# Performance work log

Measured on AMD Instinct MI355X. Metric: run time of the kernel, lower is better.

The kernel has to match this reference:

```python
import jax, jax.numpy as jnp
import numpy as np

EPS = 1e-7

def squash(t, axis=-1):
    sq = jnp.sum(jnp.square(t), axis=axis, keepdims=True)
    safe_norm = jnp.sqrt(sq + EPS)
    return t * (sq / (1.0 + sq)) / safe_norm


def setup_inputs() -> dict:
    key = jax.random.key(0)
    k1, k2 = jax.random.split(key)
    B, I, Din, N, D = 32, 1024, 32, 64, 32
    x = jax.random.normal(k1, (B, I, Din), dtype=jnp.float32)
    # glorot-ish scale ~ sqrt(2/(Din+D)) = 0.1767; use 0.1
    W = jax.random.normal(k2, (N, I, D, Din), dtype=jnp.float32) * 0.1
    return {"x": x, "W": W, "num_routing": 3}


def _infer(inputs_hat, logits):
    # softmax over the num_capsule axis (axis=1), matching tf.nn.softmax(logits, axis=1)
    route = jax.nn.softmax(logits, axis=1)                      # [B,N,1,I]
    routing = jnp.squeeze(jnp.matmul(route, inputs_hat), -2)    # [B,N,D]
    return squash(routing)


def reference(x, W, num_routing):
    # inputs_hat[b,n,i,d] = sum_k x[b,i,k] * W[n,i,d,k]
    inputs_hat = jnp.einsum('bik,nidk->bnid', x, W)             # [B,N,I,D]
    B, N, I, D = inputs_hat.shape
    ih_stop = jax.lax.stop_gradient(inputs_hat)
    logits = jnp.zeros((B, N, 1, I), dtype=inputs_hat.dtype)
    outputs = None
    for r in range(num_routing):
        if r == num_routing - 1:
            outputs = _infer(inputs_hat, logits)
        else:
            outputs = _infer(ih_stop, logits)
            # distances[b,n,1,i] = <outputs[b,n,:], ih_stop[b,n,i,:]>
            dist = jnp.matmul(outputs[:, :, None, :], jnp.swapaxes(ih_stop, -1, -2))
            logits = logits + dist
    return outputs
```

## Files before the change

kernel.cpp:

```cpp
#include <hip/hip_runtime.h>
#include <stdint.h>

#define II 1024
#define BBc 32
#define NN 64
#define DD 32
#define NDT 2048

__device__ __forceinline__ unsigned short f2bf(float f) {
  unsigned u = __float_as_uint(f);
  u += 0x7fffu + ((u >> 16) & 1u);
  return (unsigned short)(u >> 16);
}

__global__ __launch_bounds__(256) void k1_einsum(
    const float* __restrict__ x, const float* __restrict__ W,
    unsigned short* __restrict__ ih)
{
  __shared__ float xl[32][36];
  __shared__ float wl[8][256][4];
  const int t = threadIdx.x;
  const int i = blockIdx.x;
  const int half = blockIdx.y;
  const int ndg = t & 63;
  const int bg = t >> 6;
  const int b0 = bg * 8;

  {
    const int b = t >> 3, kq = (t & 7) * 4;
    const float4 v = *(const float4*)(x + ((size_t)b * II + i) * 32 + kq);
    xl[kq + 0][b] = v.x; xl[kq + 1][b] = v.y; xl[kq + 2][b] = v.z; xl[kq + 3][b] = v.w;
  }

  for (int p = 0; p < 4; ++p) {
    const int ndbase = half * 1024 + p * 256;
    __syncthreads();
#pragma unroll
    for (int it = 0; it < 8; ++it) {
      const int f = t + it * 256;
      const int kq = f & 7, nd = f >> 3;
      const int gnd = ndbase + nd;
      const int n = gnd >> 5, d = gnd & 31;
      const float4 v = *(const float4*)(W + (((size_t)n * II + i) * 32 + d) * 32 + kq * 4);
      *(float4*)&wl[kq][nd][0] = v;
    }
    __syncthreads();

    float acc[8][4] = {};
#pragma unroll
    for (int kq = 0; kq < 8; ++kq) {
      float wv[4][4];
#pragma unroll
      for (int q = 0; q < 4; ++q)
        *(float4*)wv[q] = *(const float4*)&wl[kq][ndg + 64 * q][0];
#pragma unroll
      for (int r = 0; r < 4; ++r) {
        const int k = kq * 4 + r;
        float xv[8];
        *(float4*)&xv[0] = *(const float4*)&xl[k][b0];
        *(float4*)&xv[4] = *(const float4*)&xl[k][b0 + 4];
#pragma unroll
        for (int bb = 0; bb < 8; ++bb)
#pragma unroll
          for (int q = 0; q < 4; ++q)
            acc[bb][q] += xv[bb] * wv[q][r];
      }
    }
#pragma unroll
    for (int bb = 0; bb < 8; ++bb) {
      const size_t rb = ((size_t)(b0 + bb) * II + i) * NDT + ndbase + ndg;
#pragma unroll
      for (int q = 0; q < 4; ++q)
        ih[rb + 64 * q] = f2bf(acc[bb][q]);
    }
  }
}

__global__ __launch_bounds__(256) void s0red(
    const unsigned short* __restrict__ ih, float* __restrict__ s0p)
{
  const int b = blockIdx.x, is = blockIdx.y;
  const int t = threadIdx.x;
  const unsigned short* base = ih + ((size_t)b * II + is * 64) * NDT + t * 8;
  float a[8] = {};
#pragma unroll 8
  for (int ii = 0; ii < 64; ++ii) {
    const uint4 v = *(const uint4*)(base + (size_t)ii * NDT);
    a[0] += __uint_as_float(v.x << 16); a[1] += __uint_as_float(v.x & 0xffff0000u);
    a[2] += __uint_as_float(v.y << 16); a[3] += __uint_as_float(v.y & 0xffff0000u);
    a[4] += __uint_as_float(v.z << 16); a[5] += __uint_as_float(v.z & 0xffff0000u);
    a[6] += __uint_as_float(v.w << 16); a[7] += __uint_as_float(v.w & 0xffff0000u);
  }
  float* o = s0p + ((size_t)is * BBc + b) * NDT + t * 8;
  *(float4*)(o + 0) = make_float4(a[0], a[1], a[2], a[3]);
  *(float4*)(o + 4) = make_float4(a[4], a[5], a[6], a[7]);
}

__global__ __launch_bounds__(256) void k3_route(
    const unsigned short* __restrict__ ih, const float* __restrict__ o1,
    const float* __restrict__ o2, float* __restrict__ rpart)
{
  __shared__ float red[4][NN][DD + 1];
  const int t = threadIdx.x;
  const int b = blockIdx.x, it = blockIdx.y;
  const int w = t >> 6, lane = t & 63;
  float outr[DD];
  {
    const float4* p1 = (const float4*)(o1 + ((size_t)b * NN + lane) * DD);
    if (o2 != nullptr) {
      const float4* p2 = (const float4*)(o2 + ((size_t)b * NN + lane) * DD);
#pragma unroll
      for (int q = 0; q < 8; ++q) {
        const float4 v1 = p1[q], v2 = p2[q];
        outr[q * 4 + 0] = v1.x + v2.x; outr[q * 4 + 1] = v1.y + v2.y;
        outr[q * 4 + 2] = v1.z + v2.z; outr[q * 4 + 3] = v1.w + v2.w;
      }
    } else {
#pragma unroll
      for (int q = 0; q < 8; ++q) {
        const float4 v1 = p1[q];
        outr[q * 4 + 0] = v1.x; outr[q * 4 + 1] = v1.y;
        outr[q * 4 + 2] = v1.z; outr[q * 4 + 3] = v1.w;
      }
    }
  }
  float racc[DD] = {};
  const unsigned short* ibase = ih + (size_t)b * II * NDT + lane * DD;
  for (int jj = 0; jj < 8; ++jj) {
    const int i = it * 32 + w * 8 + jj;
    const uint4* r4 = (const uint4*)(ibase + (size_t)i * NDT);
    float ihr[DD];
#pragma unroll
    for (int q = 0; q < 4; ++q) {
      const uint4 v = r4[q];
      const int d0 = q * 8;
      ihr[d0 + 0] = __uint_as_float(v.x << 16);
      ihr[d0 + 1] = __uint_as_float(v.x & 0xffff0000u);
      ihr[d0 + 2] = __uint_as_float(v.y << 16);
      ihr[d0 + 3] = __uint_as_float(v.y & 0xffff0000u);
      ihr[d0 + 4] = __uint_as_float(v.z << 16);
      ihr[d0 + 5] = __uint_as_float(v.z & 0xffff0000u);
      ihr[d0 + 6] = __uint_as_float(v.w << 16);
      ihr[d0 + 7] = __uint_as_float(v.w & 0xffff0000u);
    }
    float dist = 0.f;
#pragma unroll
    for (int d = 0; d < DD; ++d) dist += outr[d] * ihr[d];
    float m = dist;
#pragma unroll
    for (int off = 32; off > 0; off >>= 1) m = fmaxf(m, __shfl_xor(m, off));
    const float e = __expf(dist - m);
    float ss = e;
#pragma unroll
    for (int off = 32; off > 0; off >>= 1) ss += __shfl_xor(ss, off);
    const float route = e / ss;
#pragma unroll
    for (int d = 0; d < DD; ++d) racc[d] += route * ihr[d];
  }
#pragma unroll
  for (int d = 0; d < DD; ++d) red[w][lane][d] = racc[d];
  __syncthreads();
  for (int j = t; j < NN * DD; j += 256) {
    const int n = j >> 5, d = j & 31;
    const float v = red[0][n][d] + red[1][n][d] + red[2][n][d] + red[3][n][d];
    rpart[((size_t)it * BBc + b) * NDT + n * DD + d] = v;
  }
}

__global__ __launch_bounds__(256) void k_rs(
    const float* __restrict__ parts, const int nparts, const float scale,
    float* __restrict__ dst)
{
  const int b = blockIdx.x;
  const int ng = blockIdx.y;
  const int t = threadIdx.x;
  const int n = ng * 8 + (t >> 5), d = t & 31;
  const size_t off = (size_t)b * NDT + n * DD + d;
  float s = 0.f;
  for (int c = 0; c < nparts; ++c) s += parts[(size_t)c * (BBc * NDT) + off];
  s *= scale;
  float sq = s * s;
#pragma unroll
  for (int m = 16; m > 0; m >>= 1) sq += __shfl_xor(sq, m);
  const float f = sq / ((1.f + sq) * sqrtf(sq + 1e-7f));
  dst[off] = s * f;
}

extern "C" void kernel_launch(void* const* d_in, const int* in_sizes, int n_in,
                              void* d_out, int out_size, void* d_ws, size_t ws_size,
                              hipStream_t stream) {
  (void)in_sizes; (void)n_in; (void)out_size; (void)ws_size;
  const float* x = (const float*)d_in[0];
  const float* W = (const float*)d_in[1];

  char* ws = (char*)d_ws;
  unsigned short* ih = (unsigned short*)ws;
  size_t off = (size_t)BBc * II * NDT * 2;
  float* s0p = (float*)(ws + off); off += (size_t)16 * BBc * NDT * 4;
  float* rpart = (float*)(ws + off); off += (size_t)32 * BBc * NDT * 4;
  float* outA = (float*)(ws + off); off += (size_t)BBc * NDT * 4;
  float* outB = (float*)(ws + off);
  float* outF = (float*)d_out;

  k1_einsum<<<dim3(II, 2), 256, 0, stream>>>(x, W, ih);
  s0red<<<dim3(BBc, 16), 256, 0, stream>>>(ih, s0p);
  k_rs<<<dim3(BBc, 8), 256, 0, stream>>>(s0p, 16, 1.f / 64.f, outA);
  k3_route<<<dim3(BBc, 32), 256, 0, stream>>>(ih, outA, nullptr, rpart);
  k_rs<<<dim3(BBc, 8), 256, 0, stream>>>(rpart, 32, 1.f, outB);
  k3_route<<<dim3(BBc, 32), 256, 0, stream>>>(ih, outA, outB, rpart);
  k_rs<<<dim3(BBc, 8), 256, 0, stream>>>(rpart, 32, 1.f, outF);
}
```

Before: 517.1 us.

## Compute einsum with fp16 MFMA and store inputs_hat as fp16

Rewrites the first kernel to convert x and W to fp16 in registers and compute the per-i 32x2048 product with 16x16x32 MFMA instructions, staging results through LDS for coalesced stores. The intermediate inputs_hat buffer switches from bf16 to fp16, and the downstream reduction and routing kernels decode fp16 instead. This targets the FP32 FMA cost of the einsum. It reads W directly from global without LDS reuse and adds fp16 rounding of x and W, which reduces input precision.

```diff
diff --git a/kernel.cpp b/kernel.cpp
--- a/kernel.cpp
+++ b/kernel.cpp
@@ -7,89 +7,75 @@
 #define DD 32
 #define NDT 2048
 
-__device__ __forceinline__ unsigned short f2bf(float f) {
-  unsigned u = __float_as_uint(f);
-  u += 0x7fffu + ((u >> 16) & 1u);
-  return (unsigned short)(u >> 16);
+typedef _Float16 half8 __attribute__((ext_vector_type(8)));
+typedef float f32x4 __attribute__((ext_vector_type(4)));
+
+__device__ __forceinline__ half8 ld_cvt8(const float* __restrict__ p) {
+  const float4 v0 = *(const float4*)p;
+  const float4 v1 = *(const float4*)(p + 4);
+  half8 h;
+  h[0] = (_Float16)v0.x; h[1] = (_Float16)v0.y; h[2] = (_Float16)v0.z; h[3] = (_Float16)v0.w;
+  h[4] = (_Float16)v1.x; h[5] = (_Float16)v1.y; h[6] = (_Float16)v1.z; h[7] = (_Float16)v1.w;
+  return h;
 }
 
-__global__ __launch_bounds__(256) void k1_einsum(
+__global__ __launch_bounds__(256) void k1_mfma(
     const float* __restrict__ x, const float* __restrict__ W,
-    unsigned short* __restrict__ ih)
+    _Float16* __restrict__ ih)
 {
-  __shared__ float xl[32][36];
-  __shared__ float wl[8][256][4];
+  __shared__ _Float16 lbuf[4][32][64];
   const int t = threadIdx.x;
   const int i = blockIdx.x;
-  const int half = blockIdx.y;
-  const int ndg = t & 63;
-  const int bg = t >> 6;
-  const int b0 = bg * 8;
+  const int half_ = blockIdx.y;
+  const int w = t >> 6;
+  const int L = t & 63;
+  const int lm = L & 15, q = L >> 4;
 
-  {
-    const int b = t >> 3, kq = (t & 7) * 4;
-    const float4 v = *(const float4*)(x + ((size_t)b * II + i) * 32 + kq);
-    xl[kq + 0][b] = v.x; xl[kq + 1][b] = v.y; xl[kq + 2][b] = v.z; xl[kq + 3][b] = v.w;
-  }
+  half8 afrag[2];
+#pragma unroll
+  for (int mt = 0; mt < 2; ++mt)
+    afrag[mt] = ld_cvt8(x + ((size_t)(mt * 16 + lm) * II + i) * 32 + q * 8);
 
-  for (int p = 0; p < 4; ++p) {
-    const int ndbase = half * 1024 + p * 256;
+  const int ndw = half_ * 1024 + w * 256;
+  for (int g = 0; g < 4; ++g) {
+#pragma unroll
+    for (int nt = 0; nt < 4; ++nt) {
+      const int nd = ndw + g * 64 + nt * 16 + lm;
+      const int n = nd >> 5, d = nd & 31;
+      const half8 bfrag = ld_cvt8(W + (size_t)n * (II * 1024) + (size_t)i * 1024 + d * 32 + q * 8);
+      const f32x4 z = {0.f, 0.f, 0.f, 0.f};
+      f32x4 acc0 = __builtin_amdgcn_mfma_f32_16x16x32_f16(afrag[0], bfrag, z, 0, 0, 0);
+      f32x4 acc1 = __builtin_amdgcn_mfma_f32_16x16x32_f16(afrag[1], bfrag, z, 0, 0, 0);
+#pragma unroll
+      for (int r = 0; r < 4; ++r) {
+        lbuf[w][q * 4 + r][nt * 16 + lm]      = (_Float16)acc0[r];
+        lbuf[w][16 + q * 4 + r][nt * 16 + lm] = (_Float16)acc1[r];
+      }
+    }
     __syncthreads();
 #pragma unroll
-    for (int it = 0; it < 8; ++it) {
-      const int f = t + it * 256;
-      const int kq = f & 7, nd = f >> 3;
-      const int gnd = ndbase + nd;
-      const int n = gnd >> 5, d = gnd & 31;
-      const float4 v = *(const float4*)(W + (((size_t)n * II + i) * 32 + d) * 32 + kq * 4);
-      *(float4*)&wl[kq][nd][0] = v;
+    for (int j = 0; j < 4; ++j) {
+      const int row = j * 8 + (L >> 3);
+      const int ndo = (L & 7) * 8;
+      const half8 v = *(const half8*)&lbuf[w][row][ndo];
+      *(half8*)(ih + ((size_t)row * II + i) * NDT + ndw + g * 64 + ndo) = v;
     }
     __syncthreads();
-
-    float acc[8][4] = {};
-#pragma unroll
-    for (int kq = 0; kq < 8; ++kq) {
-      float wv[4][4];
-#pragma unroll
-      for (int q = 0; q < 4; ++q)
-        *(float4*)wv[q] = *(const float4*)&wl[kq][ndg + 64 * q][0];
-#pragma unroll
-      for (int r = 0; r < 4; ++r) {
-        const int k = kq * 4 + r;
-        float xv[8];
-        *(float4*)&xv[0] = *(const float4*)&xl[k][b0];
-        *(float4*)&xv[4] = *(const float4*)&xl[k][b0 + 4];
-#pragma unroll
-        for (int bb = 0; bb < 8; ++bb)
-#pragma unroll
-          for (int q = 0; q < 4; ++q)
-            acc[bb][q] += xv[bb] * wv[q][r];
-      }
-    }
-#pragma unroll
-    for (int bb = 0; bb < 8; ++bb) {
-      const size_t rb = ((size_t)(b0 + bb) * II + i) * NDT + ndbase + ndg;
-#pragma unroll
-      for (int q = 0; q < 4; ++q)
-        ih[rb + 64 * q] = f2bf(acc[bb][q]);
-    }
   }
 }
 
 __global__ __launch_bounds__(256) void s0red(
-    const unsigned short* __restrict__ ih, float* __restrict__ s0p)
+    const _Float16* __restrict__ ih, float* __restrict__ s0p)
 {
   const int b = blockIdx.x, is = blockIdx.y;
   const int t = threadIdx.x;
-  const unsigned short* base = ih + ((size_t)b * II + is * 64) * NDT + t * 8;
+  const _Float16* base = ih + ((size_t)b * II + is * 64) * NDT + t * 8;
   float a[8] = {};
 #pragma unroll 8
   for (int ii = 0; ii < 64; ++ii) {
-    const uint4 v = *(const uint4*)(base + (size_t)ii * NDT);
-    a[0] += __uint_as_float(v.x << 16); a[1] += __uint_as_float(v.x & 0xffff0000u);
-    a[2] += __uint_as_float(v.y << 16); a[3] += __uint_as_float(v.y & 0xffff0000u);
-    a[4] += __uint_as_float(v.z << 16); a[5] += __uint_as_float(v.z & 0xffff0000u);
-    a[6] += __uint_as_float(v.w << 16); a[7] += __uint_as_float(v.w & 0xffff0000u);
+    const half8 v = *(const half8*)(base + (size_t)ii * NDT);
+#pragma unroll
+    for (int j = 0; j < 8; ++j) a[j] += (float)v[j];
   }
   float* o = s0p + ((size_t)is * BBc + b) * NDT + t * 8;
   *(float4*)(o + 0) = make_float4(a[0], a[1], a[2], a[3]);
@@ -97,7 +83,7 @@
 }
 
 __global__ __launch_bounds__(256) void k3_route(
-    const unsigned short* __restrict__ ih, const float* __restrict__ o1,
+    const _Float16* __restrict__ ih, const float* __restrict__ o1,
     const float* __restrict__ o2, float* __restrict__ rpart)
 {
   __shared__ float red[4][NN][DD + 1];
@@ -110,38 +96,31 @@
     if (o2 != nullptr) {
       const float4* p2 = (const float4*)(o2 + ((size_t)b * NN + lane) * DD);
 #pragma unroll
-      for (int q = 0; q < 8; ++q) {
-        const float4 v1 = p1[q], v2 = p2[q];
-        outr[q * 4 + 0] = v1.x + v2.x; outr[q * 4 + 1] = v1.y + v2.y;
-        outr[q * 4 + 2] = v1.z + v2.z; outr[q * 4 + 3] = v1.w + v2.w;
+      for (int qq = 0; qq < 8; ++qq) {
+        const float4 v1 = p1[qq], v2 = p2[qq];
+        outr[qq * 4 + 0] = v1.x + v2.x; outr[qq * 4 + 1] = v1.y + v2.y;
+        outr[qq * 4 + 2] = v1.z + v2.z; outr[qq * 4 + 3] = v1.w + v2.w;
       }
     } else {
 #pragma unroll
-      for (int q = 0; q < 8; ++q) {
-        const float4 v1 = p1[q];
-        outr[q * 4 + 0] = v1.x; outr[q * 4 + 1] = v1.y;
-        outr[q * 4 + 2] = v1.z; outr[q * 4 + 3] = v1.w;
+      for (int qq = 0; qq < 8; ++qq) {
+        const float4 v1 = p1[qq];
+        outr[qq * 4 + 0] = v1.x; outr[qq * 4 + 1] = v1.y;
+        outr[qq * 4 + 2] = v1.z; outr[qq * 4 + 3] = v1.w;
       }
     }
   }
   float racc[DD] = {};
-  const unsigned short* ibase = ih + (size_t)b * II * NDT + lane * DD;
+  const _Float16* ibase = ih + (size_t)b * II * NDT + lane * DD;
   for (int jj = 0; jj < 8; ++jj) {
     const int i = it * 32 + w * 8 + jj;
-    const uint4* r4 = (const uint4*)(ibase + (size_t)i * NDT);
+    const half8* r8 = (const half8*)(ibase + (size_t)i * NDT);
     float ihr[DD];
 #pragma unroll
-    for (int q = 0; q < 4; ++q) {
-      const uint4 v = r4[q];
-      const int d0 = q * 8;
-      ihr[d0 + 0] = __uint_as_float(v.x << 16);
-      ihr[d0 + 1] = __uint_as_float(v.x & 0xffff0000u);
-      ihr[d0 + 2] = __uint_as_float(v.y << 16);
-      ihr[d0 + 3] = __uint_as_float(v.y & 0xffff0000u);
-      ihr[d0 + 4] = __uint_as_float(v.z << 16);
-      ihr[d0 + 5] = __uint_as_float(v.z & 0xffff0000u);
-      ihr[d0 + 6] = __uint_as_float(v.w << 16);
-      ihr[d0 + 7] = __uint_as_float(v.w & 0xffff0000u);
+    for (int qq = 0; qq < 4; ++qq) {
+      const half8 v = r8[qq];
+#pragma unroll
+      for (int j = 0; j < 8; ++j) ihr[qq * 8 + j] = (float)v[j];
     }
     float dist = 0.f;
 #pragma unroll
@@ -194,7 +173,7 @@
   const float* W = (const float*)d_in[1];
 
   char* ws = (char*)d_ws;
-  unsigned short* ih = (unsigned short*)ws;
+  _Float16* ih = (_Float16*)ws;
   size_t off = (size_t)BBc * II * NDT * 2;
   float* s0p = (float*)(ws + off); off += (size_t)16 * BBc * NDT * 4;
   float* rpart = (float*)(ws + off); off += (size_t)32 * BBc * NDT * 4;
@@ -202,7 +181,7 @@
   float* outB = (float*)(ws + off);
   float* outF = (float*)d_out;
 
-  k1_einsum<<<dim3(II, 2), 256, 0, stream>>>(x, W, ih);
+  k1_mfma<<<dim3(II, 2), 256, 0, stream>>>(x, W, ih);
   s0red<<<dim3(BBc, 16), 256, 0, stream>>>(ih, s0p);
   k_rs<<<dim3(BBc, 8), 256, 0, stream>>>(s0p, 16, 1.f / 64.f, outA);
   k3_route<<<dim3(BBc, 32), 256, 0, stream>>>(ih, outA, nullptr, rpart);
```

Measured after the change: 499.3 us. 1.04x faster.
